# Performance work log

Hardware: AMD Instinct MI355X
Metric: run time of the kernel (lower is better)

## Reference

```python
import jax, jax.numpy as jnp
import numpy as np
from jax import lax
from jax.scipy.linalg import solve_triangular

T, DX, DZ = 8192, 1024, 16
POS_CONST = 1e-6
THRESH = 1e-5


def setup_inputs() -> dict:
    key = jax.random.key(0)
    ks = jax.random.split(key, 7)
    s = 0.02  # small init scale so A ~ I and AA is well-conditioned for Cholesky
    return {
        "X": jax.random.normal(ks[0], (T, DX), jnp.float32),
        "W1": jax.random.normal(ks[1], (DX, DX), jnp.float32) * s,
        "b1": jnp.zeros((DX,), jnp.float32),
        "Wmu": jax.random.normal(ks[2], (DX, DZ), jnp.float32) * s,
        "bmu": jnp.zeros((DZ,), jnp.float32),
        "WA": jax.random.normal(ks[3], (DX, DZ * DZ), jnp.float32) * s,
        "bA": jnp.zeros((DZ * DZ,), jnp.float32),
        "WB": jax.random.normal(ks[4], (2 * DX, DZ * DZ), jnp.float32) * s,
        "bB": jnp.zeros((DZ * DZ,), jnp.float32),
        "eps": jax.random.normal(ks[5], (T, DZ), jnp.float32),
    }


def _blk_tridag_chol(AA, BB):
    # AA: (T, d, d) diagonal blocks, BB: (T-1, d, d) lower off-diagonal blocks.
    # Returns lower-bidiagonal block Cholesky: chol_A (T,d,d), chol_B (T-1,d,d).
    L0 = jnp.linalg.cholesky(AA[0])

    def step(Lprev, ins):
        Bt, At = ins
        # C = Bt @ inv(Lprev)^T, via triangular solve: Lprev C^T = Bt^T
        C = solve_triangular(Lprev, Bt.T, lower=True).T
        Lt = jnp.linalg.cholesky(At - C @ C.T)
        return Lt, (Lt, C)

    _, (Ls, Cs) = lax.scan(step, L0, (BB, AA[1:]))
    return jnp.concatenate([L0[None], Ls]), Cs


def _blk_chol_inv_identity(chol_A, chol_B):
    # Forward substitution L x = b with b = block-diagonal identity blocks.
    I = jnp.eye(DZ, dtype=chol_A.dtype)
    x0 = solve_triangular(chol_A[0], I, lower=True)

    def step(xprev, ins):
        Lt, Ct = ins
        xt = solve_triangular(Lt, I - Ct @ xprev, lower=True)
        return xt, xt

    _, xs = lax.scan(step, x0, (chol_A[1:], chol_B))
    return jnp.concatenate([x0[None], xs])


def reference(X, W1, b1, Wmu, bmu, WA, bA, WB, bB, eps):
    # encode
    h = jax.nn.relu(X @ W1 + b1)                       # (T, dx)
    mu = h @ Wmu + bmu                                 # (T, dz)
    A = (h @ WA + bA).reshape(T, DZ, DZ) + jnp.eye(DZ, dtype=X.dtype)
    hcat = jnp.concatenate([h[1:], h[:-1]], axis=1)    # (T-1, 2*dx)
    B = (hcat @ WB + bB).reshape(T - 1, DZ, DZ)

    # make_psd
    diag_sq = jnp.einsum('tij,tkj->tik', A, A)         # A A^T
    offd_sq = jnp.einsum('tij,tkj->tik', B, B)         # B B^T
    offd_sq = jnp.concatenate([jnp.zeros((1, DZ, DZ), X.dtype), offd_sq])
    AA = diag_sq + offd_sq + POS_CONST * jnp.eye(DZ, dtype=X.dtype)
    BB = jnp.einsum('tij,tkj->tik', B, A[:-1])         # B A[:-1]^T

    chol_A, chol_B = _blk_tridag_chol(AA, BB)
    r = _blk_chol_inv_identity(chol_A, chol_B)         # (T, dz, dz)

    # relu(r - thresh) + thresh == max(r, thresh)
    r = jax.nn.relu(r - THRESH) + THRESH
    logdet = -jnp.log(jnp.einsum('tii->ti', r)).sum()
    entropy = logdet + DX * T / 2.0 * (1.0 + np.log(2.0 * np.pi))

    # sample_z = mu + r^T eps per block
    sample_z = mu + jnp.einsum('tji,tj->ti', r, eps)
    return entropy, sample_z
```

## Files before the change

### kernel.cpp

```cpp
#include <hip/hip_runtime.h>
#include <math.h>


#define T_STEPS 8192
#define DXX 1024

typedef __bf16 bf16x8 __attribute__((ext_vector_type(8)));
typedef float f32x4 __attribute__((ext_vector_type(4)));
typedef unsigned short u16x8 __attribute__((ext_vector_type(8)));
typedef unsigned short u16x4 __attribute__((ext_vector_type(4)));

typedef __attribute__((address_space(1))) unsigned int as1_uint;
typedef __attribute__((address_space(3))) unsigned int as3_uint;

#define DOT4(r, b) ((r).x*(b).x + (r).y*(b).y + (r).z*(b).z + (r).w*(b).w)

__device__ __forceinline__ unsigned short f2bf(float v) {
  unsigned int u = __float_as_uint(v);
  unsigned int r = (u + 0x7FFFu + ((u >> 16) & 1u)) >> 16;
  return (unsigned short)r;
}
__device__ __forceinline__ float bf2f(unsigned short b) {
  return __uint_as_float(((unsigned int)b) << 16);
}

__device__ __forceinline__ void gload16(const unsigned short* g, unsigned short* s) {
  __builtin_amdgcn_global_load_lds((as1_uint*)g, (as3_uint*)s, 16, 0, 0);
}

__global__ __launch_bounds__(256) void prep(
    const float* __restrict__ X, unsigned short* __restrict__ Xbf,
    const float* __restrict__ W1, unsigned short* __restrict__ W1t,
    const float* __restrict__ WA, const float* __restrict__ WB,
    unsigned short* __restrict__ Wcat)
{
  int b = blockIdx.x;
  if (b < 8192) {
    int idx = b * 256 + threadIdx.x;
    float4 v = ((const float4*)X)[idx];
    u16x4 h;
    h[0] = f2bf(v.x); h[1] = f2bf(v.y); h[2] = f2bf(v.z); h[3] = f2bf(v.w);
    *(u16x4*)(Xbf + (size_t)idx * 4) = h;
    return;
  }
  __shared__ float tile[32][33];
  const float* W; unsigned short* Tt; int N, k0, n0;
  int b2 = b - 8192;
  if (b2 < 1024) {
    W = W1; Tt = W1t; N = 1024;
    k0 = (b2 & 31) * 32; n0 = (b2 >> 5) * 32;
  } else {
    int b3 = b2 - 1024;
    int sel = b3 >> 8; int r = b3 & 255;
    k0 = (r & 31) * 32; n0 = (r >> 5) * 32; N = 256;
    W = (sel == 0) ? WA : (sel == 1 ? WB : WB + 1024 * 256);
    Tt = Wcat + (size_t)sel * 256 * 1024;
  }
  int c = threadIdx.x & 31, rr = threadIdx.x >> 5;
#pragma unroll
  for (int e = 0; e < 4; ++e)
    tile[rr + 8 * e][c] = W[(size_t)(k0 + rr + 8 * e) * N + n0 + c];
  __syncthreads();
#pragma unroll
  for (int e = 0; e < 4; ++e)
    Tt[(size_t)(n0 + rr + 8 * e) * 1024 + k0 + c] = f2bf(tile[c][rr + 8 * e]);
}

#define GBK 64

__global__ __launch_bounds__(256) void gemm_mfma(
    const unsigned short* __restrict__ Abf, const unsigned short* __restrict__ Bbf,
    const float* __restrict__ bias, int biasN, float* __restrict__ outF,
    unsigned short* __restrict__ outBf, int M, int N, int K, int mode)
{
  __shared__ __align__(16) unsigned short At[128 * GBK];
  __shared__ __align__(16) unsigned short Bt[64 * GBK];
  int tid = threadIdx.x;
  int l = tid & 63;
  int w = tid >> 6;
  int wm = w >> 1, wn = w & 1;
  int lane15 = l & 15, quad = l >> 4;
  int bm = blockIdx.y * 128, bn = blockIdx.x * 64;

  int srow = (w << 3) + (l >> 3);
  int jswz = (l & 7) ^ (srow & 7);
  const unsigned short* aSrc = Abf + (size_t)(bm + srow) * K + jswz * 8;
  const unsigned short* bSrc = Bbf + (size_t)(bn + srow) * K + jswz * 8;

  f32x4 acc[4][2];
#pragma unroll
  for (int mi = 0; mi < 4; ++mi)
#pragma unroll
    for (int ni = 0; ni < 2; ++ni) acc[mi][ni] = (f32x4){0.f, 0.f, 0.f, 0.f};

  for (int k0 = 0; k0 < K; k0 += GBK) {
#pragma unroll
    for (int i = 0; i < 4; ++i)
      gload16(aSrc + (size_t)(i * 32) * K + k0, &At[(i * 32 + (w << 3)) * GBK]);
#pragma unroll
    for (int i = 0; i < 2; ++i)
      gload16(bSrc + (size_t)(i * 32) * K + k0, &Bt[(i * 32 + (w << 3)) * GBK]);
    __syncthreads();
#pragma unroll
    for (int h = 0; h < 2; ++h) {
      bf16x8 af[4], bfr[2];
#pragma unroll
      for (int mi = 0; mi < 4; ++mi) {
        int r = wm * 64 + mi * 16 + lane15;
        af[mi] = *(const bf16x8*)&At[r * GBK + ((((h << 2) + quad) ^ (lane15 & 7)) << 3)];
      }
#pragma unroll
      for (int ni = 0; ni < 2; ++ni) {
        int r = wn * 32 + ni * 16 + lane15;
        bfr[ni] = *(const bf16x8*)&Bt[r * GBK + ((((h << 2) + quad) ^ (lane15 & 7)) << 3)];
      }
#pragma unroll
      for (int mi = 0; mi < 4; ++mi)
#pragma unroll
        for (int ni = 0; ni < 2; ++ni)
          acc[mi][ni] = __builtin_amdgcn_mfma_f32_16x16x32_bf16(af[mi], bfr[ni], acc[mi][ni], 0, 0, 0);
    }
    __syncthreads();
  }

#pragma unroll
  for (int mi = 0; mi < 4; ++mi) {
#pragma unroll
    for (int ni = 0; ni < 2; ++ni) {
      int gc = bn + wn * 32 + ni * 16 + lane15;
      float bv = (bias && gc < biasN) ? bias[gc] : 0.f;
#pragma unroll
      for (int r = 0; r < 4; ++r) {
        int gr = bm + wm * 64 + mi * 16 + quad * 4 + r;
        float v = acc[mi][ni][r] + bv;
        if (mode == 1) {
          outBf[(size_t)gr * N + gc] = f2bf(fmaxf(v, 0.f));
        } else {
          outF[(size_t)gr * N + gc] = v;
        }
      }
    }
  }
}

__global__ __launch_bounds__(256) void mu_gemm(
    const unsigned short* __restrict__ hbf, const float* __restrict__ Wmu,
    const float* __restrict__ bmu, float* __restrict__ mu)
{
  int idx = blockIdx.x * 256 + threadIdx.x;
  int t = idx >> 4, j = idx & 15;
  const u16x8* ph = (const u16x8*)(hbf + (size_t)t * 1024);
  float s = bmu[j];
#pragma unroll 2
  for (int k8 = 0; k8 < 128; ++k8) {
    u16x8 hv = ph[k8];
#pragma unroll
    for (int e = 0; e < 8; ++e)
      s = fmaf(bf2f(hv[e]), Wmu[(k8 * 8 + e) * 16 + j], s);
  }
  mu[idx] = s;
}

__global__ __launch_bounds__(256) void make_psd(
    const float* __restrict__ Ccat, const float* __restrict__ bB,
    float* __restrict__ AAT, float* __restrict__ BBm, float* __restrict__ logdet,
    unsigned int* __restrict__ ticket)
{
  int t = blockIdx.x;
  int tid = threadIdx.x;
  int i = tid >> 4, j = tid & 15;
  if (t == 0 && tid == 0) { *logdet = 0.f; *ticket = 0u; }
  __shared__ float a[16][17], bp[16][17], bq[16][17];
  a[i][j] = Ccat[(size_t)t * 768 + tid] + (i == j ? 1.f : 0.f);
  bp[i][j] = (t >= 1) ? (Ccat[(size_t)t * 768 + 256 + tid] + Ccat[(size_t)(t - 1) * 768 + 512 + tid] + bB[tid]) : 0.f;
  bool has_b = (t < T_STEPS - 1);
  if (has_b) bq[i][j] = Ccat[(size_t)(t + 1) * 768 + 256 + tid] + Ccat[(size_t)t * 768 + 512 + tid] + bB[tid];
  __syncthreads();
  float s = (i == j) ? 1e-6f : 0.f;
#pragma unroll
  for (int k = 0; k < 16; ++k) s += a[i][k] * a[j][k] + bp[i][k] * bp[j][k];
  AAT[(size_t)t * 256 + ((i >> 2) * 64 + j * 4 + (i & 3))] = s;
  if (has_b) {
    float s2 = 0.f;
#pragma unroll
    for (int k = 0; k < 16; ++k) s2 += bq[i][k] * a[j][k];
    BBm[(size_t)t * 256 + tid] = s2;
  }
}

#define RIC_S 8
#define RIC_W 8
#define RIC_NCH (T_STEPS / RIC_S)

__global__ __launch_bounds__(64) void riccati_wave(
    const float* __restrict__ AAT, const float* __restrict__ BBm,
    float* __restrict__ D)
{
  int l = threadIdx.x;
  int q = l >> 4, c = l & 15;
  int p = blockIdx.x;
  int t0 = p * RIC_S;
  int tw = t0 - RIC_W; if (tw < 0) tw = 0;
  int tend = t0 + RIC_S - 1;
  int row = l >> 2, cb = (l & 3) * 4;

  __shared__ float bbs[320], dis[320], ys[320];

  float4 a4 = *(const float4*)(AAT + (size_t)tw * 256 + l * 4);
  float dr[4] = {a4.x, a4.y, a4.z, a4.w};

  float4 pbb[8], paa[8];
#pragma unroll
  for (int j = 0; j < 8; ++j) {
    pbb[j] = (float4){0.f, 0.f, 0.f, 0.f};
    paa[j] = (float4){0.f, 0.f, 0.f, 0.f};
    int t = tw + j;
    if (t < tend) {
      pbb[j] = *(const float4*)(BBm + (size_t)t * 256 + l * 4);
      paa[j] = *(const float4*)(AAT + (size_t)(t + 1) * 256 + l * 4);
    }
  }

  for (int tb = tw; tb < tend; tb += 8) {
#pragma unroll
    for (int j = 0; j < 8; ++j) {
      int t = tb + j;
      if (t < tend) {
        if (t >= t0) {
          float4 dv = {dr[0], dr[1], dr[2], dr[3]};
          *(float4*)(D + (size_t)t * 256 + l * 4) = dv;
        }
        float4 bb4 = pbb[j];
        float4 aar = paa[j];
        if (t + 8 < tend) {
          pbb[j] = *(const float4*)(BBm + (size_t)(t + 8) * 256 + l * 4);
          paa[j] = *(const float4*)(AAT + (size_t)(t + 9) * 256 + l * 4);
        }

#pragma unroll
        for (int k = 0; k < 16; ++k) {
          const int kq = k >> 2, ku = k & 3;
          float rowv = __shfl(dr[ku], (kq << 4) | c);
          float pv   = __uint_as_float(__builtin_amdgcn_readlane(__float_as_uint(dr[ku]), (kq << 4) | k));
          float cv0  = __shfl(dr[0], (l & 48) | k);
          float cv1  = __shfl(dr[1], (l & 48) | k);
          float cv2  = __shfl(dr[2], (l & 48) | k);
          float cv3  = __shfl(dr[3], (l & 48) | k);
          float rpv  = __builtin_amdgcn_rcpf(pv);
          float t1v  = rowv * rpv;
          float cva[4] = {cv0, cv1, cv2, cv3};
#pragma unroll
          for (int u = 0; u < 4; ++u) {
            bool irow = (q == kq) && (u == ku);
            float nv = irow ? ((c == k) ? rpv : t1v)
                            : ((c == k) ? (-cva[u] * rpv) : fmaf(-cva[u], t1v, dr[u]));
            dr[u] = nv;
          }
        }

        *(float4*)&bbs[row * 20 + cb] = bb4;
#pragma unroll
        for (int u = 0; u < 4; ++u) dis[(q * 4 + u) * 20 + c] = dr[u];

        float y0a = 0, y1a = 0, y2a = 0, y3a = 0;
        float y0b = 0, y1b = 0, y2b = 0, y3b = 0;
#pragma unroll
        for (int kb = 0; kb < 4; ++kb) {
          float4 bc4 = *(const float4*)&bbs[c * 20 + kb * 4];
          float4 r0 = *(const float4*)&dis[(q * 4 + 0) * 20 + kb * 4];
          float4 r1 = *(const float4*)&dis[(q * 4 + 1) * 20 + kb * 4];
          float4 r2 = *(const float4*)&dis[(q * 4 + 2) * 20 + kb * 4];
          float4 r3 = *(const float4*)&dis[(q * 4 + 3) * 20 + kb * 4];
          if (kb & 1) {
            y0b += DOT4(r0, bc4); y1b += DOT4(r1, bc4); y2b += DOT4(r2, bc4); y3b += DOT4(r3, bc4);
          } else {
            y0a += DOT4(r0, bc4); y1a += DOT4(r1, bc4); y2a += DOT4(r2, bc4); y3a += DOT4(r3, bc4);
          }
        }
        ys[(q * 4 + 0) * 20 + c] = y0a + y0b;
        ys[(q * 4 + 1) * 20 + c] = y1a + y1b;
        ys[(q * 4 + 2) * 20 + c] = y2a + y2b;
        ys[(q * 4 + 3) * 20 + c] = y3a + y3b;

        float s0a = aar.x, s1a = aar.y, s2a = aar.z, s3a = aar.w;
        float s0b = 0, s1b = 0, s2b = 0, s3b = 0;
#pragma unroll
        for (int kb = 0; kb < 4; ++kb) {
          float4 b0 = *(const float4*)&bbs[(q * 4 + 0) * 20 + kb * 4];
          float4 b1 = *(const float4*)&bbs[(q * 4 + 1) * 20 + kb * 4];
          float4 b2 = *(const float4*)&bbs[(q * 4 + 2) * 20 + kb * 4];
          float4 b3 = *(const float4*)&bbs[(q * 4 + 3) * 20 + kb * 4];
          float yk0 = ys[(kb * 4 + 0) * 20 + c];
          float yk1 = ys[(kb * 4 + 1) * 20 + c];
          float yk2 = ys[(kb * 4 + 2) * 20 + c];
          float yk3 = ys[(kb * 4 + 3) * 20 + c];
          if (kb & 1) {
            s0b -= b0.x * yk0 + b0.y * yk1 + b0.z * yk2 + b0.w * yk3;
            s1b -= b1.x * yk0 + b1.y * yk1 + b1.z * yk2 + b1.w * yk3;
            s2b -= b2.x * yk0 + b2.y * yk1 + b2.z * yk2 + b2.w * yk3;
            s3b -= b3.x * yk0 + b3.y * yk1 + b3.z * yk2 + b3.w * yk3;
          } else {
            s0a -= b0.x * yk0 + b0.y * yk1 + b0.z * yk2 + b0.w * yk3;
            s1a -= b1.x * yk0 + b1.y * yk1 + b1.z * yk2 + b1.w * yk3;
            s2a -= b2.x * yk0 + b2.y * yk1 + b2.z * yk2 + b2.w * yk3;
            s3a -= b3.x * yk0 + b3.y * yk1 + b3.z * yk2 + b3.w * yk3;
          }
        }
        dr[0] = s0a + s0b; dr[1] = s1a + s1b; dr[2] = s2a + s2b; dr[3] = s3a + s3b;
      }
    }
  }
  {
    float4 dv = {dr[0], dr[1], dr[2], dr[3]};
    *(float4*)(D + (size_t)tend * 256 + l * 4) = dv;
  }
}

__global__ __launch_bounds__(256) void chol_inv(
    const float* __restrict__ D, const float* __restrict__ BBm,
    float* __restrict__ Linv, float* __restrict__ Cmat)
{
  int t = blockIdx.x;
  int tid = threadIdx.x;
  int i = tid >> 4, j = tid & 15;
  __shared__ float d[16][17], li[16][17], bb[16][17];
  d[i][j] = D[(size_t)t * 256 + ((i >> 2) * 64 + j * 4 + (i & 3))];
  bool has_b = (t < T_STEPS - 1);
  if (has_b) bb[i][j] = BBm[(size_t)t * 256 + tid];
  float rsk[16];
  float rhsv = (i == j) ? 1.f : 0.f;
#pragma unroll
  for (int k = 0; k < 16; ++k) {
    __syncthreads();
    float dkk = d[k][k];
    float rs = 1.0f / sqrtf(dkk);
    rsk[k] = rs;
    if (j == k && i > k) d[i][k] *= rs;
    __syncthreads();
    if (i > k && j > k && j <= i) d[i][j] -= d[i][k] * d[j][k];
  }
#pragma unroll
  for (int k = 0; k < 16; ++k) {
    if (i == k) li[k][j] = rhsv * rsk[k];
    __syncthreads();
    if (i > k) rhsv -= d[i][k] * li[k][j];
  }
  Linv[(size_t)t * 256 + tid] = li[i][j];
  if (has_b) {
    float s = 0.f;
#pragma unroll
    for (int k = 0; k < 16; ++k) s += bb[i][k] * li[j][k];
    Cmat[(size_t)t * 256 + tid] = s;
  }
}

__global__ __launch_bounds__(256) void gmat_kernel(
    const float* __restrict__ Linv, const float* __restrict__ Cmat,
    float* __restrict__ Gmat)
{
  int t = blockIdx.x;
  int tid = threadIdx.x;
  int i = tid >> 4, j = tid & 15;
  if (t == 0) { Gmat[tid] = 0.f; return; }
  __shared__ float li[16][17], cm[16][17];
  li[i][j] = Linv[(size_t)t * 256 + tid];
  cm[i][j] = Cmat[(size_t)(t - 1) * 256 + tid];
  __syncthreads();
  float s = 0.f;
#pragma unroll
  for (int k = 0; k < 16; ++k) s -= li[i][k] * cm[k][j];
  Gmat[(size_t)t * 256 + tid] = s;
}

#define XS 8
#define XW 16
#define XNCH (T_STEPS / XS)

__global__ __launch_bounds__(64) void xseq_g(
    const float* __restrict__ Linv, const float* __restrict__ Gmat,
    const float* __restrict__ mu, const float* __restrict__ eps,
    float* __restrict__ out, float* __restrict__ logdet,
    unsigned int* __restrict__ ticket)
{
  int l = threadIdx.x;
  int q = l >> 4, c = l & 15;
  int p = blockIdx.x;
  int t0 = p * XS;
  int ts = t0 - XW; if (ts < 0) ts = 0;
  int tlast = t0 + XS - 1;
  int row = l >> 2, cb = (l & 3) * 4;
  __shared__ float gs[320];
  float xr[4] = {0.f, 0.f, 0.f, 0.f};
  float logacc = 0.f;

  float4 pg[8], pe[8];
  float pli[8][4], pmu[8];
#pragma unroll
  for (int j = 0; j < 8; ++j) {
    pg[j] = (float4){0.f, 0.f, 0.f, 0.f};
    pe[j] = (float4){0.f, 0.f, 0.f, 0.f};
    pli[j][0] = pli[j][1] = pli[j][2] = pli[j][3] = 0.f;
    pmu[j] = 0.f;
    int t = ts + j;
    if (t <= tlast) {
      pg[j] = *(const float4*)(Gmat + (size_t)t * 256 + l * 4);
#pragma unroll
      for (int u = 0; u < 4; ++u)
        pli[j][u] = Linv[(size_t)t * 256 + (q * 4 + u) * 16 + c];
      if (t >= t0) {
        pe[j] = *(const float4*)(eps + (size_t)t * 16 + q * 4);
        pmu[j] = mu[(size_t)t * 16 + c];
      }
    }
  }

  for (int tb = ts; tb <= tlast; tb += 8) {
#pragma unroll
    for (int j = 0; j < 8; ++j) {
      int t = tb + j;
      if (t <= tlast) {
        float4 g4 = pg[j];
        float4 e4 = pe[j];
        float muv = pmu[j];
        float li0 = pli[j][0], li1 = pli[j][1], li2 = pli[j][2], li3 = pli[j][3];
        if (t + 8 <= tlast) {
          pg[j] = *(const float4*)(Gmat + (size_t)(t + 8) * 256 + l * 4);
#pragma unroll
          for (int u = 0; u < 4; ++u)
            pli[j][u] = Linv[(size_t)(t + 8) * 256 + (q * 4 + u) * 16 + c];
          if (t + 8 >= t0) {
            pe[j] = *(const float4*)(eps + (size_t)(t + 8) * 16 + q * 4);
            pmu[j] = mu[(size_t)(t + 8) * 16 + c];
          }
        }
        *(float4*)&gs[row * 20 + cb] = g4;

        float x0a = li0, x1a = li1, x2a = li2, x3a = li3;
        float x0b = 0.f, x1b = 0.f, x2b = 0.f, x3b = 0.f;
#pragma unroll
        for (int kb = 0; kb < 4; ++kb) {
          float4 r0 = *(const float4*)&gs[(q * 4 + 0) * 20 + kb * 4];
          float4 r1 = *(const float4*)&gs[(q * 4 + 1) * 20 + kb * 4];
          float4 r2 = *(const float4*)&gs[(q * 4 + 2) * 20 + kb * 4];
          float4 r3 = *(const float4*)&gs[(q * 4 + 3) * 20 + kb * 4];
          float a0[4] = {r0.x, r0.y, r0.z, r0.w};
          float a1[4] = {r1.x, r1.y, r1.z, r1.w};
          float a2[4] = {r2.x, r2.y, r2.z, r2.w};
          float a3[4] = {r3.x, r3.y, r3.z, r3.w};
#pragma unroll
          for (int e = 0; e < 4; ++e) {
            float xk = __shfl(xr[e], (kb << 4) | c);
            if (kb & 1) {
              x0b = fmaf(a0[e], xk, x0b);
              x1b = fmaf(a1[e], xk, x1b);
              x2b = fmaf(a2[e], xk, x2b);
              x3b = fmaf(a3[e], xk, x3b);
            } else {
              x0a = fmaf(a0[e], xk, x0a);
              x1a = fmaf(a1[e], xk, x1a);
              x2a = fmaf(a2[e], xk, x2a);
              x3a = fmaf(a3[e], xk, x3a);
            }
          }
        }
        float x0 = x0a + x0b, x1 = x1a + x1b, x2 = x2a + x2b, x3 = x3a + x3b;
        xr[0] = x0; xr[1] = x1; xr[2] = x2; xr[3] = x3;

        if (t >= t0) {
          float r0v = fmaxf(x0, 1e-5f), r1v = fmaxf(x1, 1e-5f);
          float r2v = fmaxf(x2, 1e-5f), r3v = fmaxf(x3, 1e-5f);
          if (q == (c >> 2)) {
            int sel = c & 3;
            float dv = sel == 0 ? r0v : (sel == 1 ? r1v : (sel == 2 ? r2v : r3v));
            logacc -= logf(dv);
          }
          float part = r0v * e4.x + r1v * e4.y + r2v * e4.z + r3v * e4.w;
          part += __shfl_xor(part, 16);
          part += __shfl_xor(part, 32);
          if (q == 0) out[1 + (size_t)t * 16 + c] = muv + part;
        }
      }
    }
  }
#pragma unroll
  for (int off = 1; off < 64; off <<= 1) logacc += __shfl_xor(logacc, off);
  if (l == 0) {
    atomicAdd(logdet, logacc);
    __threadfence();
    unsigned int old = atomicAdd(ticket, 1u);
    if (old == XNCH - 1) {
      __threadfence();
      float ld = atomicAdd(logdet, 0.f);
      const double ENT = 0.5 * 1024.0 * 8192.0 * (1.0 + 1.8378770664093454);
      out[0] = (float)(ENT + (double)ld);
    }
  }
}

extern "C" void kernel_launch(void* const* d_in, const int* in_sizes, int n_in,
                              void* d_out, int out_size, void* d_ws, size_t ws_size,
                              hipStream_t stream)
{
  const float* X   = (const float*)d_in[0];
  const float* W1  = (const float*)d_in[1];
  const float* b1  = (const float*)d_in[2];
  const float* Wmu = (const float*)d_in[3];
  const float* bmu = (const float*)d_in[4];
  const float* WA  = (const float*)d_in[5];
  const float* bA  = (const float*)d_in[6];
  const float* WB  = (const float*)d_in[7];
  const float* bB  = (const float*)d_in[8];
  const float* eps = (const float*)d_in[9];
  float* out = (float*)d_out;
  char* ws  = (char*)d_ws;

  unsigned short* Xbf  = (unsigned short*)(ws + 0);
  unsigned short* W1t  = (unsigned short*)(ws + 16777216);
  unsigned short* hbf  = (unsigned short*)(ws + 25165824);
  unsigned short* Wcat = (unsigned short*)(ws + 50856960);
  float* Ccat   = (float*)(ws + 0);
  float* Cmat   = (float*)(ws + 0);
  float* AAT    = (float*)(ws + 25165824);
  float* Linv   = (float*)(ws + 25165824);
  float* BBp    = (float*)(ws + 33554432);
  float* Dws    = (float*)(ws + 41943040);
  float* Gmat   = (float*)(ws + 41943040);
  float* muw    = (float*)(ws + 50331648);
  float* logdet = (float*)(ws + 50855936);
  unsigned int* ticket = (unsigned int*)(ws + 50855940);

  dim3 blk(256);

  prep<<<dim3(9984), blk, 0, stream>>>(X, Xbf, W1, W1t, WA, WB, Wcat);
  gemm_mfma<<<dim3(16, 64), blk, 0, stream>>>(Xbf, W1t, b1, 1024, nullptr, hbf, 8192, 1024, 1024, 1);
  gemm_mfma<<<dim3(12, 64), blk, 0, stream>>>(hbf, Wcat, bA, 256, Ccat, nullptr, 8192, 768, 1024, 0);
  mu_gemm<<<dim3(512), blk, 0, stream>>>(hbf, Wmu, bmu, muw);
  make_psd<<<dim3(T_STEPS), blk, 0, stream>>>(Ccat, bB, AAT, BBp, logdet, ticket);
  riccati_wave<<<dim3(RIC_NCH), dim3(64), 0, stream>>>(AAT, BBp, Dws);
  chol_inv<<<dim3(T_STEPS), blk, 0, stream>>>(Dws, BBp, Linv, Cmat);
  gmat_kernel<<<dim3(T_STEPS), blk, 0, stream>>>(Linv, Cmat, Gmat);
  xseq_g<<<dim3(XNCH), dim3(64), 0, stream>>>(Linv, Gmat, muw, eps, out, logdet, ticket);
}
```

Baseline: 327.0 us.

## Rewrite chol_inv as one-wave-per-timestep with shuffles; split chunked sequential launches

chol_inv now maps one 64-lane wavefront to each 16x16 block and packs four timesteps per workgroup. It replaces the LDS plus __syncthreads Cholesky and forward substitution with register-resident rows, cross-lane shuffles and readlane. The riccati_wave and xseq_g launches are each split into two half-grid launches through a new base offset, which adds launch overhead and may change scheduling or tail behaviour. The intent is to remove barrier-heavy per-block work in chol_inv.

```diff
diff --git a/kernel.cpp b/kernel.cpp
--- a/kernel.cpp
+++ b/kernel.cpp
@@ -22,6 +22,9 @@
 }
 __device__ __forceinline__ float bf2f(unsigned short b) {
   return __uint_as_float(((unsigned int)b) << 16);
+}
+__device__ __forceinline__ float rdlane(float v, int lane) {
+  return __uint_as_float(__builtin_amdgcn_readlane(__float_as_uint(v), lane));
 }
 
 __device__ __forceinline__ void gload16(const unsigned short* g, unsigned short* s) {
@@ -194,11 +197,11 @@
 
 __global__ __launch_bounds__(64) void riccati_wave(
     const float* __restrict__ AAT, const float* __restrict__ BBm,
-    float* __restrict__ D)
+    float* __restrict__ D, int base)
 {
   int l = threadIdx.x;
   int q = l >> 4, c = l & 15;
-  int p = blockIdx.x;
+  int p = base + blockIdx.x;
   int t0 = p * RIC_S;
   int tw = t0 - RIC_W; if (tw < 0) tw = 0;
   int tend = t0 + RIC_S - 1;
@@ -241,7 +244,7 @@
         for (int k = 0; k < 16; ++k) {
           const int kq = k >> 2, ku = k & 3;
           float rowv = __shfl(dr[ku], (kq << 4) | c);
-          float pv   = __uint_as_float(__builtin_amdgcn_readlane(__float_as_uint(dr[ku]), (kq << 4) | k));
+          float pv   = rdlane(dr[ku], (kq << 4) | k);
           float cv0  = __shfl(dr[0], (l & 48) | k);
           float cv1  = __shfl(dr[1], (l & 48) | k);
           float cv2  = __shfl(dr[2], (l & 48) | k);
@@ -320,37 +323,90 @@
     const float* __restrict__ D, const float* __restrict__ BBm,
     float* __restrict__ Linv, float* __restrict__ Cmat)
 {
-  int t = blockIdx.x;
   int tid = threadIdx.x;
-  int i = tid >> 4, j = tid & 15;
-  __shared__ float d[16][17], li[16][17], bb[16][17];
-  d[i][j] = D[(size_t)t * 256 + ((i >> 2) * 64 + j * 4 + (i & 3))];
+  int wv = tid >> 6, l = tid & 63;
+  int t = blockIdx.x * 4 + wv;
+  int q = l >> 4, c = l & 15;
+
+  __shared__ float lds[4][640];
+  float* bbs = &lds[wv][0];
+  float* lis = &lds[wv][320];
+
+  float4 a4 = *(const float4*)(D + (size_t)t * 256 + l * 4);
+  float a[4] = {a4.x, a4.y, a4.z, a4.w};
+  float4 bb4 = *(const float4*)(BBm + (size_t)t * 256 + l * 4);
   bool has_b = (t < T_STEPS - 1);
-  if (has_b) bb[i][j] = BBm[(size_t)t * 256 + tid];
+
   float rsk[16];
-  float rhsv = (i == j) ? 1.f : 0.f;
 #pragma unroll
   for (int k = 0; k < 16; ++k) {
-    __syncthreads();
-    float dkk = d[k][k];
+    const int kq = k >> 2, ku = k & 3;
+    float dkk = rdlane(a[ku], (kq << 4) | k);
     float rs = 1.0f / sqrtf(dkk);
     rsk[k] = rs;
-    if (j == k && i > k) d[i][k] *= rs;
-    __syncthreads();
-    if (i > k && j > k && j <= i) d[i][j] -= d[i][k] * d[j][k];
-  }
+#pragma unroll
+    for (int u = 0; u < 4; ++u) {
+      int i = q * 4 + u;
+      if (c == k && i > k) a[u] *= rs;
+    }
+    float Lik[4];
+#pragma unroll
+    for (int u = 0; u < 4; ++u) Lik[u] = __shfl(a[u], (l & 48) | k);
+    float t0 = __shfl(a[0], ((c >> 2) << 4) | k);
+    float t1 = __shfl(a[1], ((c >> 2) << 4) | k);
+    float t2 = __shfl(a[2], ((c >> 2) << 4) | k);
+    float t3 = __shfl(a[3], ((c >> 2) << 4) | k);
+    int sel = c & 3;
+    float Ljk = sel == 0 ? t0 : (sel == 1 ? t1 : (sel == 2 ? t2 : t3));
+#pragma unroll
+    for (int u = 0; u < 4; ++u) {
+      int i = q * 4 + u;
+      if (i > k && c > k) a[u] = fmaf(-Lik[u], Ljk, a[u]);
+    }
+  }
+
+  float r[4], x[4];
+#pragma unroll
+  for (int u = 0; u < 4; ++u) { r[u] = (q * 4 + u == c) ? 1.f : 0.f; x[u] = 0.f; }
 #pragma unroll
   for (int k = 0; k < 16; ++k) {
-    if (i == k) li[k][j] = rhsv * rsk[k];
-    __syncthreads();
-    if (i > k) rhsv -= d[i][k] * li[k][j];
-  }
-  Linv[(size_t)t * 256 + tid] = li[i][j];
+    const int kq = k >> 2, ku = k & 3;
+    if (q == kq) x[ku] = r[ku] * rsk[k];
+    float xkc = __shfl(x[ku], (kq << 4) | c);
+    float Lik[4];
+#pragma unroll
+    for (int u = 0; u < 4; ++u) Lik[u] = __shfl(a[u], (l & 48) | k);
+#pragma unroll
+    for (int u = 0; u < 4; ++u) {
+      int i = q * 4 + u;
+      if (i > k) r[u] = fmaf(-Lik[u], xkc, r[u]);
+    }
+  }
+
+#pragma unroll
+  for (int u = 0; u < 4; ++u)
+    Linv[(size_t)t * 256 + (q * 4 + u) * 16 + c] = x[u];
+
   if (has_b) {
-    float s = 0.f;
-#pragma unroll
-    for (int k = 0; k < 16; ++k) s += bb[i][k] * li[j][k];
-    Cmat[(size_t)t * 256 + tid] = s;
+    *(float4*)&bbs[(l >> 2) * 20 + (l & 3) * 4] = bb4;
+#pragma unroll
+    for (int u = 0; u < 4; ++u) lis[(q * 4 + u) * 20 + c] = x[u];
+    float cacc[4] = {0.f, 0.f, 0.f, 0.f};
+#pragma unroll
+    for (int kb = 0; kb < 4; ++kb) {
+      float4 lc = *(const float4*)&lis[c * 20 + kb * 4];
+      float4 b0 = *(const float4*)&bbs[(q * 4 + 0) * 20 + kb * 4];
+      float4 b1 = *(const float4*)&bbs[(q * 4 + 1) * 20 + kb * 4];
+      float4 b2 = *(const float4*)&bbs[(q * 4 + 2) * 20 + kb * 4];
+      float4 b3 = *(const float4*)&bbs[(q * 4 + 3) * 20 + kb * 4];
+      cacc[0] += DOT4(b0, lc);
+      cacc[1] += DOT4(b1, lc);
+      cacc[2] += DOT4(b2, lc);
+      cacc[3] += DOT4(b3, lc);
+    }
+#pragma unroll
+    for (int u = 0; u < 4; ++u)
+      Cmat[(size_t)t * 256 + (q * 4 + u) * 16 + c] = cacc[u];
   }
 }
 
@@ -380,11 +436,11 @@
     const float* __restrict__ Linv, const float* __restrict__ Gmat,
     const float* __restrict__ mu, const float* __restrict__ eps,
     float* __restrict__ out, float* __restrict__ logdet,
-    unsigned int* __restrict__ ticket)
+    unsigned int* __restrict__ ticket, int base)
 {
   int l = threadIdx.x;
   int q = l >> 4, c = l & 15;
-  int p = blockIdx.x;
+  int p = base + blockIdx.x;
   int t0 = p * XS;
   int ts = t0 - XW; if (ts < 0) ts = 0;
   int tlast = t0 + XS - 1;
@@ -536,8 +592,10 @@
   gemm_mfma<<<dim3(12, 64), blk, 0, stream>>>(hbf, Wcat, bA, 256, Ccat, nullptr, 8192, 768, 1024, 0);
   mu_gemm<<<dim3(512), blk, 0, stream>>>(hbf, Wmu, bmu, muw);
   make_psd<<<dim3(T_STEPS), blk, 0, stream>>>(Ccat, bB, AAT, BBp, logdet, ticket);
-  riccati_wave<<<dim3(RIC_NCH), dim3(64), 0, stream>>>(AAT, BBp, Dws);
-  chol_inv<<<dim3(T_STEPS), blk, 0, stream>>>(Dws, BBp, Linv, Cmat);
+  riccati_wave<<<dim3(RIC_NCH / 2), dim3(64), 0, stream>>>(AAT, BBp, Dws, 0);
+  riccati_wave<<<dim3(RIC_NCH / 2), dim3(64), 0, stream>>>(AAT, BBp, Dws, RIC_NCH / 2);
+  chol_inv<<<dim3(T_STEPS / 4), blk, 0, stream>>>(Dws, BBp, Linv, Cmat);
   gmat_kernel<<<dim3(T_STEPS), blk, 0, stream>>>(Linv, Cmat, Gmat);
-  xseq_g<<<dim3(XNCH), dim3(64), 0, stream>>>(Linv, Gmat, muw, eps, out, logdet, ticket);
-}
+  xseq_g<<<dim3(XNCH / 2), dim3(64), 0, stream>>>(Linv, Gmat, muw, eps, out, logdet, ticket, 0);
+  xseq_g<<<dim3(XNCH / 2), dim3(64), 0, stream>>>(Linv, Gmat, muw, eps, out, logdet, ticket, XNCH / 2);
+}
```

After: 355.9 us. 8.8% more time.
